# Optimization experiments

Measured on AMD Instinct MI355X. Metric: run time of the kernel, lower is better.

## Reference

```python
import jax, jax.numpy as jnp
import numpy as np

N_NODES = 2176
N_IN = 64
N_HID = 2048
N_OUT = 64
NODE_DIM = 64
HEADS = 4


def _build_edge_index():
    hs, os_ = N_IN, N_IN + N_HID
    # input -> hidden block (order: for i: for h)
    s1 = np.repeat(np.arange(0, N_IN), N_HID)
    t1 = np.tile(np.arange(hs, os_), N_IN)
    # hidden -> output block (order: for h: for o)
    s2 = np.repeat(np.arange(hs, os_), N_OUT)
    t2 = np.tile(np.arange(os_, N_NODES), N_HID)
    return jnp.asarray(np.stack([np.concatenate([s1, s2]), np.concatenate([t1, t2])]), dtype=jnp.int32)


def setup_inputs() -> dict:
    key = jax.random.key(0)
    ks = jax.random.split(key, 20)
    D, H = NODE_DIM, HEADS
    edge_index = _build_edge_index()  # [2, E]
    E = edge_index.shape[1]

    def xavier(k, shape):
        fan_in, fan_out = shape[0], shape[1]
        lim = float(np.sqrt(6.0 / (fan_in + fan_out)))
        return jax.random.uniform(k, shape, jnp.float32, -lim, lim)

    return {
        "x_input": jax.random.normal(ks[0], (N_IN,), jnp.float32),
        "node_features": jax.random.normal(ks[1], (N_NODES, D), jnp.float32) * 0.1,
        "edge_weights": jax.random.normal(ks[2], (E, 1), jnp.float32) * 0.1,
        "edge_index": edge_index,
        "wq1": xavier(ks[3], (D, D * H)), "wk1": xavier(ks[4], (D, D * H)),
        "wv1": xavier(ks[5], (D, D * H)), "we1": xavier(ks[6], (1, H)),
        "wo1": xavier(ks[7], (D * H, D)), "bo1": jnp.zeros((D,), jnp.float32),
        "wq2": xavier(ks[8], (D, D * H)), "wk2": xavier(ks[9], (D, D * H)),
        "wv2": xavier(ks[10], (D, D * H)), "we2": xavier(ks[11], (1, H)),
        "wo2": xavier(ks[12], (D * H, D)), "bo2": jnp.zeros((D,), jnp.float32),
        "wproj": xavier(ks[13], (D, 1)), "bproj": jnp.zeros((1,), jnp.float32),
        "num_output_nodes": N_OUT,
    }


def _message_pass(x, edge_index, ew, wq, wk, wv, we, wo, bo):
    # x: [N, D_in]; edge_index: [2, E]; ew: [E, 1]
    src, tgt = edge_index[0], edge_index[1]
    dout = wo.shape[1]
    heads = wq.shape[1] // dout
    q = (x[tgt] @ wq).reshape(-1, heads, dout)  # [E, H, D]
    k = (x[src] @ wk).reshape(-1, heads, dout)
    v = (x[src] @ wv).reshape(-1, heads, dout)
    attn = (q * k).sum(-1) / jnp.sqrt(jnp.float32(dout)) + ew @ we  # [E, H]
    # NOTE: the per-target segment-softmax in the torch source is dead code;
    # the effective math is leaky_relu then a global softmax over edges.
    attn = jax.nn.leaky_relu(attn, negative_slope=0.2)
    attn = jax.nn.softmax(attn, axis=0)
    weighted_v = (attn[:, :, None] * v).reshape(-1, heads * dout)  # [E, H*D]
    out = jax.ops.segment_sum(weighted_v, tgt, num_segments=x.shape[0])  # [N, H*D]
    out = out @ wo + bo
    return out + x  # residual (in_channels == out_channels)


def reference(x_input, node_features, edge_weights, edge_index,
              wq1, wk1, wv1, we1, wo1, bo1,
              wq2, wk2, wv2, we2, wo2, bo2,
              wproj, bproj, num_output_nodes):
    n_in = x_input.shape[0]
    x = node_features.at[:n_in, 0].set(x_input)
    x = jax.nn.relu(_message_pass(x, edge_index, edge_weights, wq1, wk1, wv1, we1, wo1, bo1))
    x = jax.nn.relu(_message_pass(x, edge_index, edge_weights, wq2, wk2, wv2, we2, wo2, bo2))
    out_nodes = x[x.shape[0] - num_output_nodes:]
    output = jax.nn.sigmoid(out_nodes @ wproj + bproj).squeeze()
    return output, x
```

## Files before the change

kernel.cpp:

```cpp
#include <hip/hip_runtime.h>
#include <math.h>

#define E1 131072

__device__ __forceinline__ void gemm_nn_acc(const float* __restrict__ A,
                                            const float* __restrict__ B,
                                            float acc[4][4], int tr, int tc) {
  for (int k4 = 0; k4 < 16; ++k4) {
    float4 b0 = *(const float4*)&B[(k4 * 4 + 0) * 68 + tc * 4];
    float4 b1 = *(const float4*)&B[(k4 * 4 + 1) * 68 + tc * 4];
    float4 b2 = *(const float4*)&B[(k4 * 4 + 2) * 68 + tc * 4];
    float4 b3 = *(const float4*)&B[(k4 * 4 + 3) * 68 + tc * 4];
#pragma unroll
    for (int a = 0; a < 4; ++a) {
      float4 av = *(const float4*)&A[(tr + 16 * a) * 68 + k4 * 4];
      acc[a][0] += av.x * b0.x + av.y * b1.x + av.z * b2.x + av.w * b3.x;
      acc[a][1] += av.x * b0.y + av.y * b1.y + av.z * b2.y + av.w * b3.y;
      acc[a][2] += av.x * b0.z + av.y * b1.z + av.z * b2.z + av.w * b3.z;
      acc[a][3] += av.x * b0.w + av.y * b1.w + av.z * b2.w + av.w * b3.w;
    }
  }
}

__device__ __forceinline__ void gemm_nt_acc(const float* __restrict__ A,
                                            const float* __restrict__ B,
                                            float acc[4][4], int tr, int tc) {
  for (int k4 = 0; k4 < 16; ++k4) {
    float4 av[4], bv[4];
#pragma unroll
    for (int a = 0; a < 4; ++a) av[a] = *(const float4*)&A[(tr + 16 * a) * 68 + k4 * 4];
#pragma unroll
    for (int b = 0; b < 4; ++b) bv[b] = *(const float4*)&B[(tc + 16 * b) * 68 + k4 * 4];
#pragma unroll
    for (int a = 0; a < 4; ++a)
#pragma unroll
      for (int b = 0; b < 4; ++b)
        acc[a][b] += av[a].x * bv[b].x + av[a].y * bv[b].y +
                     av[a].z * bv[b].z + av[a].w * bv[b].w;
  }
}

__device__ __forceinline__ void st_tile(float* __restrict__ C, const float acc[4][4],
                                        int tr, int tc) {
#pragma unroll
  for (int a = 0; a < 4; ++a)
    *(float4*)&C[(tr + 16 * a) * 68 + tc * 4] =
        make_float4(acc[a][0], acc[a][1], acc[a][2], acc[a][3]);
}

__device__ __forceinline__ void ld_x(float* __restrict__ dst, const float* __restrict__ src,
                                     int tid, bool sub, const float* __restrict__ xinp) {
  for (int t4 = tid; t4 < 1024; t4 += 256) {
    int r = t4 >> 4, c0 = (t4 & 15) * 4;
    float4 v = *(const float4*)(src + t4 * 4);
    if (sub && c0 == 0) v.x = xinp[r];
    *(float4*)&dst[r * 68 + c0] = v;
  }
}

__device__ __forceinline__ void ld_w(float* __restrict__ dst, const float* __restrict__ w,
                                     int h, int tid) {
  for (int t4 = tid; t4 < 1024; t4 += 256) {
    int k = t4 >> 4, c0 = (t4 & 15) * 4;
    *(float4*)&dst[k * 68 + c0] = *(const float4*)(w + k * 256 + h * 64 + c0);
  }
}

__global__ __launch_bounds__(256) void k_attn1(const float* __restrict__ x,
                                               const float* __restrict__ xinp,
                                               const float* __restrict__ wq1,
                                               const float* __restrict__ wk1,
                                               const float* __restrict__ we1,
                                               const float* __restrict__ ew,
                                               const float* __restrict__ wq2,
                                               const float* __restrict__ wk2,
                                               const float* __restrict__ wv1,
                                               const float* __restrict__ wo1,
                                               const float* __restrict__ wv2,
                                               const float* __restrict__ wo2,
                                               float* __restrict__ AggH,
                                               float* __restrict__ part,
                                               float* __restrict__ bsum,
                                               float* __restrict__ Mb,
                                               float* __restrict__ W2b) {
  __shared__ float A[4352];
  __shared__ float B[4352];
  __shared__ float C[4352];
  __shared__ float D[4352];
  __shared__ float Ew[4352];
  __shared__ float F[4352];
  __shared__ float G[4352];
  __shared__ float wred[4];
  const int bid = blockIdx.x, tid = threadIdx.x;
  const bool r1 = bid < 128;
  const int tile = (r1 ? bid : bid - 128) >> 2;
  const int h = bid & 3;
  const int j0 = tile * 64;
  const int rowSrc = r1 ? 0 : (64 + j0);
  const int rowQ = r1 ? (64 + j0) : 2112;
  const int tr = tid >> 4, tc = tid & 15;
  const float weh = we1[h];

  ld_x(A, x + rowSrc * 64, tid, r1, xinp);
  ld_x(B, x + rowQ * 64, tid, false, nullptr);
  ld_w(Ew, wk1, h, tid);
  ld_w(F, wq1, h, tid);
  if (r1) {
    for (int t4 = tid; t4 < 1024; t4 += 256) {
      int i = t4 >> 4, jl0 = (t4 & 15) * 4;
      *(float4*)&G[i * 68 + jl0] = *(const float4*)(ew + i * 2048 + j0 + jl0);
    }
  } else {
    for (int t4 = tid; t4 < 1024; t4 += 256) {
      int jl = t4 >> 4, o0 = (t4 & 15) * 4;
      *(float4*)&G[jl * 68 + o0] = *(const float4*)(ew + E1 + (j0 + jl) * 64 + o0);
    }
  }
  __syncthreads();

  {
    float kt[4][4];
#pragma unroll
    for (int a = 0; a < 4; ++a)
#pragma unroll
      for (int q = 0; q < 4; ++q) kt[a][q] = 0.f;
    gemm_nn_acc(A, Ew, kt, tr, tc);
    st_tile(C, kt, tr, tc);
    float qt[4][4];
#pragma unroll
    for (int a = 0; a < 4; ++a)
#pragma unroll
      for (int q = 0; q < 4; ++q) qt[a][q] = 0.f;
    gemm_nn_acc(B, F, qt, tr, tc);
    st_tile(D, qt, tr, tc);
  }
  __syncthreads();

  float acc[4][4];
#pragma unroll
  for (int a = 0; a < 4; ++a)
#pragma unroll
    for (int b = 0; b < 4; ++b) acc[a][b] = 0.f;
  gemm_nt_acc(D, C, acc, tr, tc);
  float esum = 0.f;
#pragma unroll
  for (int a = 0; a < 4; ++a) {
    int row = tr + 16 * a;
#pragma unroll
    for (int b = 0; b < 4; ++b) {
      int col = tc + 16 * b;
      float v = acc[a][b] * 0.125f + G[col * 68 + row] * weh;
      v = (v >= 0.f) ? v : 0.2f * v;
      v = fminf(v, 60.f);
      float e = __expf(v);
      esum += e;
      B[row * 68 + col] = e;
    }
  }
#pragma unroll
  for (int s = 1; s < 64; s <<= 1) esum += __shfl_xor(esum, s);
  if ((tid & 63) == 0) wred[tid >> 6] = esum;
  __syncthreads();

  float u[4][4];
#pragma unroll
  for (int a = 0; a < 4; ++a)
#pragma unroll
    for (int q = 0; q < 4; ++q) u[a][q] = 0.f;
  gemm_nn_acc(B, A, u, tr, tc);
  if (r1) {
#pragma unroll
    for (int a = 0; a < 4; ++a)
      *(float4*)&AggH[(j0 + tr + 16 * a) * 256 + h * 64 + tc * 4] =
          make_float4(u[a][0], u[a][1], u[a][2], u[a][3]);
  } else {
#pragma unroll
    for (int a = 0; a < 4; ++a)
      *(float4*)&part[tile * 16384 + (tr + 16 * a) * 256 + h * 64 + tc * 4] =
          make_float4(u[a][0], u[a][1], u[a][2], u[a][3]);
  }
  if (tid == 0) bsum[bid] = (wred[0] + wred[1]) + (wred[2] + wred[3]);

  if (bid < 12) {
    __syncthreads();
    const int type = bid >> 2, hh = bid & 3;
    if (type == 0) {
      for (int t4 = tid; t4 < 1024; t4 += 256) {
        int r = t4 >> 4, c0 = (t4 & 15) * 4;
        *(float4*)&A[r * 68 + c0] = *(const float4*)(wq2 + r * 256 + hh * 64 + c0);
        *(float4*)&B[r * 68 + c0] = *(const float4*)(wk2 + r * 256 + hh * 64 + c0);
      }
      __syncthreads();
      float m[4][4];
#pragma unroll
      for (int a = 0; a < 4; ++a)
#pragma unroll
        for (int b = 0; b < 4; ++b) m[a][b] = 0.f;
      gemm_nt_acc(A, B, m, tr, tc);
#pragma unroll
      for (int a = 0; a < 4; ++a)
#pragma unroll
        for (int b = 0; b < 4; ++b)
          Mb[hh * 4096 + (tr + 16 * a) * 64 + tc + 16 * b] = m[a][b];
    } else {
      const float* wv = (type == 1) ? wv1 : wv2;
      const float* wo = (type == 1) ? wo1 : wo2;
      for (int t4 = tid; t4 < 1024; t4 += 256) {
        int r = t4 >> 4, c0 = (t4 & 15) * 4;
        *(float4*)&A[r * 68 + c0] = *(const float4*)(wv + r * 256 + hh * 64 + c0);
        *(float4*)&B[r * 68 + c0] = *(const float4*)(wo + (hh * 64 + r) * 64 + c0);
      }
      __syncthreads();
      float m[4][4];
#pragma unroll
      for (int a = 0; a < 4; ++a)
#pragma unroll
        for (int b = 0; b < 4; ++b) m[a][b] = 0.f;
      gemm_nn_acc(A, B, m, tr, tc);
      float* o = W2b + (type - 1) * 16384;
#pragma unroll
      for (int a = 0; a < 4; ++a)
        *(float4*)&o[(hh * 64 + tr + 16 * a) * 64 + tc * 4] =
            make_float4(m[a][0], m[a][1], m[a][2], m[a][3]);
    }
  }
}

__global__ __launch_bounds__(256) void k_attn2(const float* __restrict__ x,
                                               const float* __restrict__ Mb,
                                               const float* __restrict__ we,
                                               const float* __restrict__ ew,
                                               float* __restrict__ AggH,
                                               float* __restrict__ part,
                                               float* __restrict__ bsum) {
  __shared__ float A[4352];
  __shared__ float B[4352];
  __shared__ float C[4352];
  __shared__ float D[4352];
  __shared__ float Em[4352];
  __shared__ float wred[4];
  const int bid = blockIdx.x, tid = threadIdx.x;
  const bool r1 = bid < 128;
  const int tile = (r1 ? bid : bid - 128) >> 2;
  const int h = bid & 3;
  const int j0 = tile * 64;
  const int rowSrc = r1 ? 0 : (64 + j0);
  const int rowQ = r1 ? (64 + j0) : 2112;
  const int tr = tid >> 4, tc = tid & 15;
  const float weh = we[h];
  const float* Mh = Mb + h * 4096;

  ld_x(A, x + rowSrc * 64, tid, false, nullptr);
  ld_x(B, x + rowQ * 64, tid, false, nullptr);
  for (int t4 = tid; t4 < 1024; t4 += 256) {
    int r = t4 >> 4, c0 = (t4 & 15) * 4;
    *(float4*)&Em[r * 68 + c0] = *(const float4*)(Mh + r * 64 + c0);
  }
  if (r1) {
    for (int t4 = tid; t4 < 1024; t4 += 256) {
      int i = t4 >> 4, jl0 = (t4 & 15) * 4;
      *(float4*)&D[i * 68 + jl0] = *(const float4*)(ew + i * 2048 + j0 + jl0);
    }
  } else {
    for (int t4 = tid; t4 < 1024; t4 += 256) {
      int jl = t4 >> 4, o0 = (t4 & 15) * 4;
      *(float4*)&D[jl * 68 + o0] = *(const float4*)(ew + E1 + (j0 + jl) * 64 + o0);
    }
  }
  __syncthreads();

  {
    float t_[4][4];
#pragma unroll
    for (int a = 0; a < 4; ++a)
#pragma unroll
      for (int q = 0; q < 4; ++q) t_[a][q] = 0.f;
    gemm_nn_acc(B, Em, t_, tr, tc);
    st_tile(C, t_, tr, tc);
  }
  __syncthreads();

  float acc[4][4];
#pragma unroll
  for (int a = 0; a < 4; ++a)
#pragma unroll
    for (int b = 0; b < 4; ++b) acc[a][b] = 0.f;
  gemm_nt_acc(C, A, acc, tr, tc);
  float esum = 0.f;
#pragma unroll
  for (int a = 0; a < 4; ++a) {
    int row = tr + 16 * a;
#pragma unroll
    for (int b = 0; b < 4; ++b) {
      int col = tc + 16 * b;
      float v = acc[a][b] * 0.125f + D[col * 68 + row] * weh;
      v = (v >= 0.f) ? v : 0.2f * v;
      v = fminf(v, 60.f);
      float e = __expf(v);
      esum += e;
      B[row * 68 + col] = e;
    }
  }
#pragma unroll
  for (int s = 1; s < 64; s <<= 1) esum += __shfl_xor(esum, s);
  if ((tid & 63) == 0) wred[tid >> 6] = esum;
  __syncthreads();

  float u[4][4];
#pragma unroll
  for (int a = 0; a < 4; ++a)
#pragma unroll
    for (int q = 0; q < 4; ++q) u[a][q] = 0.f;
  gemm_nn_acc(B, A, u, tr, tc);
  if (r1) {
#pragma unroll
    for (int a = 0; a < 4; ++a)
      *(float4*)&AggH[(j0 + tr + 16 * a) * 256 + h * 64 + tc * 4] =
          make_float4(u[a][0], u[a][1], u[a][2], u[a][3]);
  } else {
#pragma unroll
    for (int a = 0; a < 4; ++a)
      *(float4*)&part[tile * 16384 + (tr + 16 * a) * 256 + h * 64 + tc * 4] =
          make_float4(u[a][0], u[a][1], u[a][2], u[a][3]);
  }
  if (tid == 0) bsum[bid] = (wred[0] + wred[1]) + (wred[2] + wred[3]);
}

template<bool SUB, bool HEAD>
__global__ __launch_bounds__(256) void k_proj(const float* __restrict__ xin,
                                              const float* __restrict__ xinp,
                                              const float* __restrict__ AggH,
                                              const float* __restrict__ part,
                                              const float* __restrict__ bsum,
                                              const float* __restrict__ W2,
                                              const float* __restrict__ bo,
                                              const float* __restrict__ wproj,
                                              const float* __restrict__ bproj,
                                              float* __restrict__ xout,
                                              float* __restrict__ outh) {
  __shared__ float As[4][260];
  const int bid = blockIdx.x, tid = threadIdx.x;
  const int n0 = bid * 4;
  const int nl = tid >> 6, d = tid & 63;
  const int node = n0 + nl;

  float inv[4];
  {
    int l = tid & 63;
#pragma unroll
    for (int hh = 0; hh < 4; ++hh) {
      float s = (l < 32) ? bsum[l * 4 + hh] : bsum[128 + (l - 32) * 4 + hh];
#pragma unroll
      for (int st = 1; st < 64; st <<= 1) s += __shfl_xor(s, st);
      inv[hh] = 1.f / s;
    }
  }

  float xres = xin[node * 64 + d];
  if (SUB) {
    if (d == 0 && node < 64) xres = xinp[node];
  }

  float val;
  if (n0 < 64) {
    val = xres + bo[d];
  } else {
    if (n0 < 2112) {
      int a = tid >> 6, c0 = (tid & 63) * 4;
      float4 v = *(const float4*)&AggH[(n0 - 64 + a) * 256 + c0];
      float iv = inv[c0 >> 6];
      *(float4*)&As[a][c0] = make_float4(v.x * iv, v.y * iv, v.z * iv, v.w * iv);
    } else {
      int a = tid >> 6, c0 = (tid & 63) * 4;
      float4 s = make_float4(0.f, 0.f, 0.f, 0.f);
      for (int ch = 0; ch < 32; ++ch) {
        float4 v = *(const float4*)&part[ch * 16384 + (n0 - 2112 + a) * 256 + c0];
        s.x += v.x; s.y += v.y; s.z += v.z; s.w += v.w;
      }
      float iv = inv[c0 >> 6];
      *(float4*)&As[a][c0] = make_float4(s.x * iv, s.y * iv, s.z * iv, s.w * iv);
    }
    __syncthreads();
    float acc = xres + bo[d];
    for (int c4 = 0; c4 < 64; ++c4) {
      float4 a4 = *(const float4*)&As[nl][c4 * 4];
      acc += a4.x * W2[(c4 * 4 + 0) * 64 + d] + a4.y * W2[(c4 * 4 + 1) * 64 + d] +
             a4.z * W2[(c4 * 4 + 2) * 64 + d] + a4.w * W2[(c4 * 4 + 3) * 64 + d];
    }
    val = acc;
  }
  val = fmaxf(val, 0.f);
  xout[node * 64 + d] = val;

  if (HEAD) {
    if (n0 >= 2112) {
      float wv = val * wproj[d];
#pragma unroll
      for (int st = 1; st < 64; st <<= 1) wv += __shfl_xor(wv, st);
      if ((tid & 63) == 0) outh[node - 2112] = 1.f / (1.f + __expf(-(wv + bproj[0])));
    }
  }
}

extern "C" void kernel_launch(void* const* d_in, const int* in_sizes, int n_in,
                              void* d_out, int out_size, void* d_ws, size_t ws_size,
                              hipStream_t stream) {
  const float* x_input       = (const float*)d_in[0];
  const float* node_features = (const float*)d_in[1];
  const float* edge_weights  = (const float*)d_in[2];
  const float* wq1 = (const float*)d_in[4];
  const float* wk1 = (const float*)d_in[5];
  const float* wv1 = (const float*)d_in[6];
  const float* we1 = (const float*)d_in[7];
  const float* wo1 = (const float*)d_in[8];
  const float* bo1 = (const float*)d_in[9];
  const float* wq2 = (const float*)d_in[10];
  const float* wk2 = (const float*)d_in[11];
  const float* wv2 = (const float*)d_in[12];
  const float* we2 = (const float*)d_in[13];
  const float* wo2 = (const float*)d_in[14];
  const float* bo2 = (const float*)d_in[15];
  const float* wproj = (const float*)d_in[16];
  const float* bproj = (const float*)d_in[17];

  float* out = (float*)d_out;
  float* ws = (float*)d_ws;
  float* xB   = ws;
  float* AggH = xB + 139264;
  float* part = AggH + 524288;
  float* bsum = part + 524288;
  float* Mb   = bsum + 256;
  float* W2b  = Mb + 16384;

  k_attn1<<<256, 256, 0, stream>>>(node_features, x_input, wq1, wk1, we1, edge_weights,
                                   wq2, wk2, wv1, wo1, wv2, wo2,
                                   AggH, part, bsum, Mb, W2b);
  k_proj<true, false><<<544, 256, 0, stream>>>(node_features, x_input, AggH, part, bsum,
                                               W2b, bo1, nullptr, nullptr, xB, nullptr);
  k_attn2<<<256, 256, 0, stream>>>(xB, Mb, we2, edge_weights, AggH, part, bsum);
  k_proj<false, true><<<544, 256, 0, stream>>>(xB, nullptr, AggH, part, bsum,
                                               W2b + 16384, bo2, wproj, bproj, out + 64, out);
}
```

Baseline: 58.15 us.

## Halve hidden-node tile size to double attention blocks and read weights from global

The attention kernels now tile 32 hidden nodes per block instead of 64, which doubles the grid from 256 to 512 blocks so more of the GPU's compute units are busy. Weight matrices (wq/wk/Mb) are read directly from global memory inside the GEMM rather than staged in LDS, and the shared arrays are merged into one smaller buffer, cutting LDS use per block to raise occupancy. In exchange, k_proj must reduce 64 partial chunks instead of 32, partial-sum workspace doubles, and global weight reads may repeat across threads.

```diff
diff --git a/kernel.cpp b/kernel.cpp
--- a/kernel.cpp
+++ b/kernel.cpp
@@ -3,16 +3,17 @@
 
 #define E1 131072
 
-__device__ __forceinline__ void gemm_nn_acc(const float* __restrict__ A,
+template<int AR, int K4>
+__device__ __forceinline__ void gemm_nn_lds(const float* __restrict__ A,
                                             const float* __restrict__ B,
-                                            float acc[4][4], int tr, int tc) {
-  for (int k4 = 0; k4 < 16; ++k4) {
+                                            float acc[AR][4], int tr, int tc) {
+  for (int k4 = 0; k4 < K4; ++k4) {
     float4 b0 = *(const float4*)&B[(k4 * 4 + 0) * 68 + tc * 4];
     float4 b1 = *(const float4*)&B[(k4 * 4 + 1) * 68 + tc * 4];
     float4 b2 = *(const float4*)&B[(k4 * 4 + 2) * 68 + tc * 4];
     float4 b3 = *(const float4*)&B[(k4 * 4 + 3) * 68 + tc * 4];
 #pragma unroll
-    for (int a = 0; a < 4; ++a) {
+    for (int a = 0; a < AR; ++a) {
       float4 av = *(const float4*)&A[(tr + 16 * a) * 68 + k4 * 4];
       acc[a][0] += av.x * b0.x + av.y * b1.x + av.z * b2.x + av.w * b3.x;
       acc[a][1] += av.x * b0.y + av.y * b1.y + av.z * b2.y + av.w * b3.y;
@@ -22,48 +23,52 @@
   }
 }
 
-__device__ __forceinline__ void gemm_nt_acc(const float* __restrict__ A,
+template<int AR, int K4>
+__device__ __forceinline__ void gemm_nn_g(const float* __restrict__ A,
+                                          const float* __restrict__ Bg, int ldb,
+                                          float acc[AR][4], int tr, int tc) {
+  for (int k4 = 0; k4 < K4; ++k4) {
+    float4 b0 = *(const float4*)(Bg + (k4 * 4 + 0) * ldb + tc * 4);
+    float4 b1 = *(const float4*)(Bg + (k4 * 4 + 1) * ldb + tc * 4);
+    float4 b2 = *(const float4*)(Bg + (k4 * 4 + 2) * ldb + tc * 4);
+    float4 b3 = *(const float4*)(Bg + (k4 * 4 + 3) * ldb + tc * 4);
+#pragma unroll
+    for (int a = 0; a < AR; ++a) {
+      float4 av = *(const float4*)&A[(tr + 16 * a) * 68 + k4 * 4];
+      acc[a][0] += av.x * b0.x + av.y * b1.x + av.z * b2.x + av.w * b3.x;
+      acc[a][1] += av.x * b0.y + av.y * b1.y + av.z * b2.y + av.w * b3.y;
+      acc[a][2] += av.x * b0.z + av.y * b1.z + av.z * b2.z + av.w * b3.z;
+      acc[a][3] += av.x * b0.w + av.y * b1.w + av.z * b2.w + av.w * b3.w;
+    }
+  }
+}
+
+template<int AR, int BR>
+__device__ __forceinline__ void gemm_nt_lds(const float* __restrict__ A,
                                             const float* __restrict__ B,
-                                            float acc[4][4], int tr, int tc) {
+                                            float acc[AR][BR], int tr, int tc) {
   for (int k4 = 0; k4 < 16; ++k4) {
-    float4 av[4], bv[4];
-#pragma unroll
-    for (int a = 0; a < 4; ++a) av[a] = *(const float4*)&A[(tr + 16 * a) * 68 + k4 * 4];
-#pragma unroll
-    for (int b = 0; b < 4; ++b) bv[b] = *(const float4*)&B[(tc + 16 * b) * 68 + k4 * 4];
-#pragma unroll
-    for (int a = 0; a < 4; ++a)
-#pragma unroll
-      for (int b = 0; b < 4; ++b)
+    float4 av[AR], bv[BR];
+#pragma unroll
+    for (int a = 0; a < AR; ++a) av[a] = *(const float4*)&A[(tr + 16 * a) * 68 + k4 * 4];
+#pragma unroll
+    for (int b = 0; b < BR; ++b) bv[b] = *(const float4*)&B[(tc + 16 * b) * 68 + k4 * 4];
+#pragma unroll
+    for (int a = 0; a < AR; ++a)
+#pragma unroll
+      for (int b = 0; b < BR; ++b)
         acc[a][b] += av[a].x * bv[b].x + av[a].y * bv[b].y +
                      av[a].z * bv[b].z + av[a].w * bv[b].w;
   }
 }
 
-__device__ __forceinline__ void st_tile(float* __restrict__ C, const float acc[4][4],
+template<int AR>
+__device__ __forceinline__ void st_tile(float* __restrict__ C, const float acc[AR][4],
                                         int tr, int tc) {
 #pragma unroll
-  for (int a = 0; a < 4; ++a)
+  for (int a = 0; a < AR; ++a)
     *(float4*)&C[(tr + 16 * a) * 68 + tc * 4] =
         make_float4(acc[a][0], acc[a][1], acc[a][2], acc[a][3]);
-}
-
-__device__ __forceinline__ void ld_x(float* __restrict__ dst, const float* __restrict__ src,
-                                     int tid, bool sub, const float* __restrict__ xinp) {
-  for (int t4 = tid; t4 < 1024; t4 += 256) {
-    int r = t4 >> 4, c0 = (t4 & 15) * 4;
-    float4 v = *(const float4*)(src + t4 * 4);
-    if (sub && c0 == 0) v.x = xinp[r];
-    *(float4*)&dst[r * 68 + c0] = v;
-  }
-}
-
-__device__ __forceinline__ void ld_w(float* __restrict__ dst, const float* __restrict__ w,
-                                     int h, int tid) {
-  for (int t4 = tid; t4 < 1024; t4 += 256) {
-    int k = t4 >> 4, c0 = (t4 & 15) * 4;
-    *(float4*)&dst[k * 68 + c0] = *(const float4*)(w + k * 256 + h * 64 + c0);
-  }
 }
 
 __global__ __launch_bounds__(256) void k_attn1(const float* __restrict__ x,
@@ -83,146 +88,206 @@
                                                float* __restrict__ bsum,
                                                float* __restrict__ Mb,
                                                float* __restrict__ W2b) {
-  __shared__ float A[4352];
-  __shared__ float B[4352];
-  __shared__ float C[4352];
-  __shared__ float D[4352];
-  __shared__ float Ew[4352];
-  __shared__ float F[4352];
-  __shared__ float G[4352];
+  __shared__ float S_[17408];
   __shared__ float wred[4];
   const int bid = blockIdx.x, tid = threadIdx.x;
-  const bool r1 = bid < 128;
-  const int tile = (r1 ? bid : bid - 128) >> 2;
+  const bool r1 = bid < 256;
+  const int tile = (r1 ? bid : bid - 256) >> 2;
   const int h = bid & 3;
-  const int j0 = tile * 64;
-  const int rowSrc = r1 ? 0 : (64 + j0);
-  const int rowQ = r1 ? (64 + j0) : 2112;
+  const int j0 = tile * 32;
   const int tr = tid >> 4, tc = tid & 15;
   const float weh = we1[h];
 
-  ld_x(A, x + rowSrc * 64, tid, r1, xinp);
-  ld_x(B, x + rowQ * 64, tid, false, nullptr);
-  ld_w(Ew, wk1, h, tid);
-  ld_w(F, wq1, h, tid);
   if (r1) {
+    float* A = S_;
+    float* B = S_ + 4352;
+    float* C = S_ + 6528;
+    float* D = S_ + 10880;
+    float* G = S_ + 13056;
     for (int t4 = tid; t4 < 1024; t4 += 256) {
-      int i = t4 >> 4, jl0 = (t4 & 15) * 4;
+      int r = t4 >> 4, c0 = (t4 & 15) * 4;
+      float4 v = *(const float4*)(x + t4 * 4);
+      if (c0 == 0) v.x = xinp[r];
+      *(float4*)&A[r * 68 + c0] = v;
+    }
+    for (int t4 = tid; t4 < 512; t4 += 256) {
+      int r = t4 >> 4, c0 = (t4 & 15) * 4;
+      *(float4*)&B[r * 68 + c0] = *(const float4*)(x + (64 + j0 + r) * 64 + c0);
+    }
+    for (int t4 = tid; t4 < 512; t4 += 256) {
+      int i = t4 >> 3, jl0 = (t4 & 7) * 4;
       *(float4*)&G[i * 68 + jl0] = *(const float4*)(ew + i * 2048 + j0 + jl0);
     }
+    __syncthreads();
+    {
+      float kt[4][4];
+#pragma unroll
+      for (int a = 0; a < 4; ++a)
+#pragma unroll
+        for (int q = 0; q < 4; ++q) kt[a][q] = 0.f;
+      gemm_nn_g<4, 16>(A, wk1 + h * 64, 256, kt, tr, tc);
+      st_tile<4>(C, kt, tr, tc);
+      float qt[2][4];
+#pragma unroll
+      for (int a = 0; a < 2; ++a)
+#pragma unroll
+        for (int q = 0; q < 4; ++q) qt[a][q] = 0.f;
+      gemm_nn_g<2, 16>(B, wq1 + h * 64, 256, qt, tr, tc);
+      st_tile<2>(D, qt, tr, tc);
+    }
+    __syncthreads();
+    float lg[2][4];
+#pragma unroll
+    for (int a = 0; a < 2; ++a)
+#pragma unroll
+      for (int b = 0; b < 4; ++b) lg[a][b] = 0.f;
+    gemm_nt_lds<2, 4>(D, C, lg, tr, tc);
+    float esum = 0.f;
+#pragma unroll
+    for (int a = 0; a < 2; ++a) {
+      int row = tr + 16 * a;
+#pragma unroll
+      for (int b = 0; b < 4; ++b) {
+        int col = tc + 16 * b;
+        float v = lg[a][b] * 0.125f + G[col * 68 + row] * weh;
+        v = (v >= 0.f) ? v : 0.2f * v;
+        v = fminf(v, 60.f);
+        float e = __expf(v);
+        esum += e;
+        B[row * 68 + col] = e;
+      }
+    }
+#pragma unroll
+    for (int s = 1; s < 64; s <<= 1) esum += __shfl_xor(esum, s);
+    if ((tid & 63) == 0) wred[tid >> 6] = esum;
+    __syncthreads();
+    float u[2][4];
+#pragma unroll
+    for (int a = 0; a < 2; ++a)
+#pragma unroll
+      for (int q = 0; q < 4; ++q) u[a][q] = 0.f;
+    gemm_nn_lds<2, 16>(B, A, u, tr, tc);
+#pragma unroll
+    for (int a = 0; a < 2; ++a)
+      *(float4*)&AggH[(j0 + tr + 16 * a) * 256 + h * 64 + tc * 4] =
+          make_float4(u[a][0], u[a][1], u[a][2], u[a][3]);
+    if (tid == 0) bsum[bid] = (wred[0] + wred[1]) + (wred[2] + wred[3]);
+
+    if (bid < 12) {
+      __syncthreads();
+      const int type = bid >> 2, hh = bid & 3;
+      if (type == 0) {
+        for (int t4 = tid; t4 < 1024; t4 += 256) {
+          int k = t4 >> 4, c0 = (t4 & 15) * 4;
+          *(float4*)&A[k * 68 + c0] = *(const float4*)(wq2 + k * 256 + hh * 64 + c0);
+          *(float4*)&C[k * 68 + c0] = *(const float4*)(wk2 + k * 256 + hh * 64 + c0);
+        }
+        __syncthreads();
+        float m[4][4];
+#pragma unroll
+        for (int a = 0; a < 4; ++a)
+#pragma unroll
+          for (int b = 0; b < 4; ++b) m[a][b] = 0.f;
+        gemm_nt_lds<4, 4>(A, C, m, tr, tc);
+#pragma unroll
+        for (int a = 0; a < 4; ++a)
+#pragma unroll
+          for (int b = 0; b < 4; ++b)
+            Mb[hh * 4096 + (tr + 16 * a) * 64 + tc + 16 * b] = m[a][b];
+      } else {
+        const float* wv = (type == 1) ? wv1 : wv2;
+        const float* wo = (type == 1) ? wo1 : wo2;
+        for (int t4 = tid; t4 < 1024; t4 += 256) {
+          int k = t4 >> 4, c0 = (t4 & 15) * 4;
+          *(float4*)&A[k * 68 + c0] = *(const float4*)(wv + k * 256 + hh * 64 + c0);
+          *(float4*)&C[k * 68 + c0] = *(const float4*)(wo + (hh * 64 + k) * 64 + c0);
+        }
+        __syncthreads();
+        float m[4][4];
+#pragma unroll
+        for (int a = 0; a < 4; ++a)
+#pragma unroll
+          for (int q = 0; q < 4; ++q) m[a][q] = 0.f;
+        gemm_nn_lds<4, 16>(A, C, m, tr, tc);
+        float* o = W2b + (type - 1) * 16384;
+#pragma unroll
+        for (int a = 0; a < 4; ++a)
+          *(float4*)&o[(hh * 64 + tr + 16 * a) * 64 + tc * 4] =
+              make_float4(m[a][0], m[a][1], m[a][2], m[a][3]);
+      }
+    }
   } else {
+    float* A = S_;
+    float* B = S_ + 2176;
+    float* C = S_ + 6528;
+    float* D = S_ + 8704;
+    float* G = S_ + 13056;
+    for (int t4 = tid; t4 < 512; t4 += 256) {
+      int r = t4 >> 4, c0 = (t4 & 15) * 4;
+      *(float4*)&A[r * 68 + c0] = *(const float4*)(x + (64 + j0 + r) * 64 + c0);
+    }
     for (int t4 = tid; t4 < 1024; t4 += 256) {
+      int r = t4 >> 4, c0 = (t4 & 15) * 4;
+      *(float4*)&B[r * 68 + c0] = *(const float4*)(x + (2112 + r) * 64 + c0);
+    }
+    for (int t4 = tid; t4 < 512; t4 += 256) {
       int jl = t4 >> 4, o0 = (t4 & 15) * 4;
       *(float4*)&G[jl * 68 + o0] = *(const float4*)(ew + E1 + (j0 + jl) * 64 + o0);
     }
-  }
-  __syncthreads();
-
-  {
-    float kt[4][4];
+    __syncthreads();
+    {
+      float kt[2][4];
+#pragma unroll
+      for (int a = 0; a < 2; ++a)
+#pragma unroll
+        for (int q = 0; q < 4; ++q) kt[a][q] = 0.f;
+      gemm_nn_g<2, 16>(A, wk1 + h * 64, 256, kt, tr, tc);
+      st_tile<2>(C, kt, tr, tc);
+      float qt[4][4];
+#pragma unroll
+      for (int a = 0; a < 4; ++a)
+#pragma unroll
+        for (int q = 0; q < 4; ++q) qt[a][q] = 0.f;
+      gemm_nn_g<4, 16>(B, wq1 + h * 64, 256, qt, tr, tc);
+      st_tile<4>(D, qt, tr, tc);
+    }
+    __syncthreads();
+    float lg[4][2];
 #pragma unroll
     for (int a = 0; a < 4; ++a)
 #pragma unroll
-      for (int q = 0; q < 4; ++q) kt[a][q] = 0.f;
-    gemm_nn_acc(A, Ew, kt, tr, tc);
-    st_tile(C, kt, tr, tc);
-    float qt[4][4];
+      for (int b = 0; b < 2; ++b) lg[a][b] = 0.f;
+    gemm_nt_lds<4, 2>(D, C, lg, tr, tc);
+    float esum = 0.f;
+#pragma unroll
+    for (int a = 0; a < 4; ++a) {
+      int row = tr + 16 * a;
+#pragma unroll
+      for (int b = 0; b < 2; ++b) {
+        int col = tc + 16 * b;
+        float v = lg[a][b] * 0.125f + G[col * 68 + row] * weh;
+        v = (v >= 0.f) ? v : 0.2f * v;
+        v = fminf(v, 60.f);
+        float e = __expf(v);
+        esum += e;
+        B[row * 68 + col] = e;
+      }
+    }
+#pragma unroll
+    for (int s = 1; s < 64; s <<= 1) esum += __shfl_xor(esum, s);
+    if ((tid & 63) == 0) wred[tid >> 6] = esum;
+    __syncthreads();
+    float u[4][4];
 #pragma unroll
     for (int a = 0; a < 4; ++a)
 #pragma unroll
-      for (int q = 0; q < 4; ++q) qt[a][q] = 0.f;
-    gemm_nn_acc(B, F, qt, tr, tc);
-    st_tile(D, qt, tr, tc);
-  }
-  __syncthreads();
-
-  float acc[4][4];
-#pragma unroll
-  for (int a = 0; a < 4; ++a)
-#pragma unroll
-    for (int b = 0; b < 4; ++b) acc[a][b] = 0.f;
-  gemm_nt_acc(D, C, acc, tr, tc);
-  float esum = 0.f;
-#pragma unroll
-  for (int a = 0; a < 4; ++a) {
-    int row = tr + 16 * a;
-#pragma unroll
-    for (int b = 0; b < 4; ++b) {
-      int col = tc + 16 * b;
-      float v = acc[a][b] * 0.125f + G[col * 68 + row] * weh;
-      v = (v >= 0.f) ? v : 0.2f * v;
-      v = fminf(v, 60.f);
-      float e = __expf(v);
-      esum += e;
-      B[row * 68 + col] = e;
-    }
-  }
-#pragma unroll
-  for (int s = 1; s < 64; s <<= 1) esum += __shfl_xor(esum, s);
-  if ((tid & 63) == 0) wred[tid >> 6] = esum;
-  __syncthreads();
-
-  float u[4][4];
-#pragma unroll
-  for (int a = 0; a < 4; ++a)
-#pragma unroll
-    for (int q = 0; q < 4; ++q) u[a][q] = 0.f;
-  gemm_nn_acc(B, A, u, tr, tc);
-  if (r1) {
-#pragma unroll
-    for (int a = 0; a < 4; ++a)
-      *(float4*)&AggH[(j0 + tr + 16 * a) * 256 + h * 64 + tc * 4] =
-          make_float4(u[a][0], u[a][1], u[a][2], u[a][3]);
-  } else {
+      for (int q = 0; q < 4; ++q) u[a][q] = 0.f;
+    gemm_nn_lds<4, 8>(B, A, u, tr, tc);
 #pragma unroll
     for (int a = 0; a < 4; ++a)
       *(float4*)&part[tile * 16384 + (tr + 16 * a) * 256 + h * 64 + tc * 4] =
           make_float4(u[a][0], u[a][1], u[a][2], u[a][3]);
-  }
-  if (tid == 0) bsum[bid] = (wred[0] + wred[1]) + (wred[2] + wred[3]);
-
-  if (bid < 12) {
-    __syncthreads();
-    const int type = bid >> 2, hh = bid & 3;
-    if (type == 0) {
-      for (int t4 = tid; t4 < 1024; t4 += 256) {
-        int r = t4 >> 4, c0 = (t4 & 15) * 4;
-        *(float4*)&A[r * 68 + c0] = *(const float4*)(wq2 + r * 256 + hh * 64 + c0);
-        *(float4*)&B[r * 68 + c0] = *(const float4*)(wk2 + r * 256 + hh * 64 + c0);
-      }
-      __syncthreads();
-      float m[4][4];
-#pragma unroll
-      for (int a = 0; a < 4; ++a)
-#pragma unroll
-        for (int b = 0; b < 4; ++b) m[a][b] = 0.f;
-      gemm_nt_acc(A, B, m, tr, tc);
-#pragma unroll
-      for (int a = 0; a < 4; ++a)
-#pragma unroll
-        for (int b = 0; b < 4; ++b)
-          Mb[hh * 4096 + (tr + 16 * a) * 64 + tc + 16 * b] = m[a][b];
-    } else {
-      const float* wv = (type == 1) ? wv1 : wv2;
-      const float* wo = (type == 1) ? wo1 : wo2;
-      for (int t4 = tid; t4 < 1024; t4 += 256) {
-        int r = t4 >> 4, c0 = (t4 & 15) * 4;
-        *(float4*)&A[r * 68 + c0] = *(const float4*)(wv + r * 256 + hh * 64 + c0);
-        *(float4*)&B[r * 68 + c0] = *(const float4*)(wo + (hh * 64 + r) * 64 + c0);
-      }
-      __syncthreads();
-      float m[4][4];
-#pragma unroll
-      for (int a = 0; a < 4; ++a)
-#pragma unroll
-        for (int b = 0; b < 4; ++b) m[a][b] = 0.f;
-      gemm_nn_acc(A, B, m, tr, tc);
-      float* o = W2b + (type - 1) * 16384;
-#pragma unroll
-      for (int a = 0; a < 4; ++a)
-        *(float4*)&o[(hh * 64 + tr + 16 * a) * 64 + tc * 4] =
-            make_float4(m[a][0], m[a][1], m[a][2], m[a][3]);
-    }
+    if (tid == 0) bsum[bid] = (wred[0] + wred[1]) + (wred[2] + wred[3]);
   }
 }
 
@@ -233,97 +298,146 @@
                                                float* __restrict__ AggH,
                                                float* __restrict__ part,
                                                float* __restrict__ bsum) {
-  __shared__ float A[4352];
-  __shared__ float B[4352];
-  __shared__ float C[4352];
-  __shared__ float D[4352];
-  __shared__ float Em[4352];
+  __shared__ float S_[13056];
   __shared__ float wred[4];
   const int bid = blockIdx.x, tid = threadIdx.x;
-  const bool r1 = bid < 128;
-  const int tile = (r1 ? bid : bid - 128) >> 2;
+  const bool r1 = bid < 256;
+  const int tile = (r1 ? bid : bid - 256) >> 2;
   const int h = bid & 3;
-  const int j0 = tile * 64;
-  const int rowSrc = r1 ? 0 : (64 + j0);
-  const int rowQ = r1 ? (64 + j0) : 2112;
+  const int j0 = tile * 32;
   const int tr = tid >> 4, tc = tid & 15;
   const float weh = we[h];
   const float* Mh = Mb + h * 4096;
 
-  ld_x(A, x + rowSrc * 64, tid, false, nullptr);
-  ld_x(B, x + rowQ * 64, tid, false, nullptr);
-  for (int t4 = tid; t4 < 1024; t4 += 256) {
-    int r = t4 >> 4, c0 = (t4 & 15) * 4;
-    *(float4*)&Em[r * 68 + c0] = *(const float4*)(Mh + r * 64 + c0);
-  }
   if (r1) {
+    float* A = S_;
+    float* B = S_ + 4352;
+    float* C = S_ + 6528;
+    float* G = S_ + 8704;
     for (int t4 = tid; t4 < 1024; t4 += 256) {
-      int i = t4 >> 4, jl0 = (t4 & 15) * 4;
-      *(float4*)&D[i * 68 + jl0] = *(const float4*)(ew + i * 2048 + j0 + jl0);
-    }
-  } else {
-    for (int t4 = tid; t4 < 1024; t4 += 256) {
-      int jl = t4 >> 4, o0 = (t4 & 15) * 4;
-      *(float4*)&D[jl * 68 + o0] = *(const float4*)(ew + E1 + (j0 + jl) * 64 + o0);
-    }
-  }
-  __syncthreads();
-
-  {
-    float t_[4][4];
-#pragma unroll
-    for (int a = 0; a < 4; ++a)
-#pragma unroll
-      for (int q = 0; q < 4; ++q) t_[a][q] = 0.f;
-    gemm_nn_acc(B, Em, t_, tr, tc);
-    st_tile(C, t_, tr, tc);
-  }
-  __syncthreads();
-
-  float acc[4][4];
-#pragma unroll
-  for (int a = 0; a < 4; ++a)
-#pragma unroll
-    for (int b = 0; b < 4; ++b) acc[a][b] = 0.f;
-  gemm_nt_acc(C, A, acc, tr, tc);
-  float esum = 0.f;
-#pragma unroll
-  for (int a = 0; a < 4; ++a) {
-    int row = tr + 16 * a;
-#pragma unroll
-    for (int b = 0; b < 4; ++b) {
-      int col = tc + 16 * b;
-      float v = acc[a][b] * 0.125f + D[col * 68 + row] * weh;
-      v = (v >= 0.f) ? v : 0.2f * v;
-      v = fminf(v, 60.f);
-      float e = __expf(v);
-      esum += e;
-      B[row * 68 + col] = e;
-    }
-  }
-#pragma unroll
-  for (int s = 1; s < 64; s <<= 1) esum += __shfl_xor(esum, s);
-  if ((tid & 63) == 0) wred[tid >> 6] = esum;
-  __syncthreads();
-
-  float u[4][4];
-#pragma unroll
-  for (int a = 0; a < 4; ++a)
-#pragma unroll
-    for (int q = 0; q < 4; ++q) u[a][q] = 0.f;
-  gemm_nn_acc(B, A, u, tr, tc);
-  if (r1) {
-#pragma unroll
-    for (int a = 0; a < 4; ++a)
+      int r = t4 >> 4, c0 = (t4 & 15) * 4;
+      *(float4*)&A[r * 68 + c0] = *(const float4*)(x + t4 * 4);
+    }
+    for (int t4 = tid; t4 < 512; t4 += 256) {
+      int r = t4 >> 4, c0 = (t4 & 15) * 4;
+      *(float4*)&B[r * 68 + c0] = *(const float4*)(x + (64 + j0 + r) * 64 + c0);
+    }
+    for (int t4 = tid; t4 < 512; t4 += 256) {
+      int i = t4 >> 3, jl0 = (t4 & 7) * 4;
+      *(float4*)&G[i * 68 + jl0] = *(const float4*)(ew + i * 2048 + j0 + jl0);
+    }
+    __syncthreads();
+    {
+      float t_[2][4];
+#pragma unroll
+      for (int a = 0; a < 2; ++a)
+#pragma unroll
+        for (int q = 0; q < 4; ++q) t_[a][q] = 0.f;
+      gemm_nn_g<2, 16>(B, Mh, 64, t_, tr, tc);
+      st_tile<2>(C, t_, tr, tc);
+    }
+    __syncthreads();
+    float lg[2][4];
+#pragma unroll
+    for (int a = 0; a < 2; ++a)
+#pragma unroll
+      for (int b = 0; b < 4; ++b) lg[a][b] = 0.f;
+    gemm_nt_lds<2, 4>(C, A, lg, tr, tc);
+    float esum = 0.f;
+#pragma unroll
+    for (int a = 0; a < 2; ++a) {
+      int row = tr + 16 * a;
+#pragma unroll
+      for (int b = 0; b < 4; ++b) {
+        int col = tc + 16 * b;
+        float v = lg[a][b] * 0.125f + G[col * 68 + row] * weh;
+        v = (v >= 0.f) ? v : 0.2f * v;
+        v = fminf(v, 60.f);
+        float e = __expf(v);
+        esum += e;
+        B[row * 68 + col] = e;
+      }
+    }
+#pragma unroll
+    for (int s = 1; s < 64; s <<= 1) esum += __shfl_xor(esum, s);
+    if ((tid & 63) == 0) wred[tid >> 6] = esum;
+    __syncthreads();
+    float u[2][4];
+#pragma unroll
+    for (int a = 0; a < 2; ++a)
+#pragma unroll
+      for (int q = 0; q < 4; ++q) u[a][q] = 0.f;
+    gemm_nn_lds<2, 16>(B, A, u, tr, tc);
+#pragma unroll
+    for (int a = 0; a < 2; ++a)
       *(float4*)&AggH[(j0 + tr + 16 * a) * 256 + h * 64 + tc * 4] =
           make_float4(u[a][0], u[a][1], u[a][2], u[a][3]);
+    if (tid == 0) bsum[bid] = (wred[0] + wred[1]) + (wred[2] + wred[3]);
   } else {
+    float* A = S_;
+    float* B = S_ + 2176;
+    float* C = S_ + 6528;
+    float* G = S_ + 10880;
+    for (int t4 = tid; t4 < 512; t4 += 256) {
+      int r = t4 >> 4, c0 = (t4 & 15) * 4;
+      *(float4*)&A[r * 68 + c0] = *(const float4*)(x + (64 + j0 + r) * 64 + c0);
+    }
+    for (int t4 = tid; t4 < 1024; t4 += 256) {
+      int r = t4 >> 4, c0 = (t4 & 15) * 4;
+      *(float4*)&B[r * 68 + c0] = *(const float4*)(x + (2112 + r) * 64 + c0);
+    }
+    for (int t4 = tid; t4 < 512; t4 += 256) {
+      int jl = t4 >> 4, o0 = (t4 & 15) * 4;
+      *(float4*)&G[jl * 68 + o0] = *(const float4*)(ew + E1 + (j0 + jl) * 64 + o0);
+    }
+    __syncthreads();
+    {
+      float t_[4][4];
+#pragma unroll
+      for (int a = 0; a < 4; ++a)
+#pragma unroll
+        for (int q = 0; q < 4; ++q) t_[a][q] = 0.f;
+      gemm_nn_g<4, 16>(B, Mh, 64, t_, tr, tc);
+      st_tile<4>(C, t_, tr, tc);
+    }
+    __syncthreads();
+    float lg[4][2];
+#pragma unroll
+    for (int a = 0; a < 4; ++a)
+#pragma unroll
+      for (int b = 0; b < 2; ++b) lg[a][b] = 0.f;
+    gemm_nt_lds<4, 2>(C, A, lg, tr, tc);
+    float esum = 0.f;
+#pragma unroll
+    for (int a = 0; a < 4; ++a) {
+      int row = tr + 16 * a;
+#pragma unroll
+      for (int b = 0; b < 2; ++b) {
+        int col = tc + 16 * b;
+        float v = lg[a][b] * 0.125f + G[col * 68 + row] * weh;
+        v = (v >= 0.f) ? v : 0.2f * v;
+        v = fminf(v, 60.f);
+        float e = __expf(v);
+        esum += e;
+        B[row * 68 + col] = e;
+      }
+    }
+#pragma unroll
+    for (int s = 1; s < 64; s <<= 1) esum += __shfl_xor(esum, s);
+    if ((tid & 63) == 0) wred[tid >> 6] = esum;
+    __syncthreads();
+    float u[4][4];
+#pragma unroll
+    for (int a = 0; a < 4; ++a)
+#pragma unroll
+      for (int q = 0; q < 4; ++q) u[a][q] = 0.f;
+    gemm_nn_lds<4, 8>(B, A, u, tr, tc);
 #pragma unroll
     for (int a = 0; a < 4; ++a)
       *(float4*)&part[tile * 16384 + (tr + 16 * a) * 256 + h * 64 + tc * 4] =
           make_float4(u[a][0], u[a][1], u[a][2], u[a][3]);
-  }
-  if (tid == 0) bsum[bid] = (wred[0] + wred[1]) + (wred[2] + wred[3]);
+    if (tid == 0) bsum[bid] = (wred[0] + wred[1]) + (wred[2] + wred[3]);
+  }
 }
 
 template<bool SUB, bool HEAD>
@@ -349,7 +463,7 @@
     int l = tid & 63;
 #pragma unroll
     for (int hh = 0; hh < 4; ++hh) {
-      float s = (l < 32) ? bsum[l * 4 + hh] : bsum[128 + (l - 32) * 4 + hh];
+      float s = bsum[4 * l + hh] + bsum[256 + 4 * l + hh];
 #pragma unroll
       for (int st = 1; st < 64; st <<= 1) s += __shfl_xor(s, st);
       inv[hh] = 1.f / s;
@@ -373,7 +487,7 @@
     } else {
       int a = tid >> 6, c0 = (tid & 63) * 4;
       float4 s = make_float4(0.f, 0.f, 0.f, 0.f);
-      for (int ch = 0; ch < 32; ++ch) {
+      for (int ch = 0; ch < 64; ++ch) {
         float4 v = *(const float4*)&part[ch * 16384 + (n0 - 2112 + a) * 256 + c0];
         s.x += v.x; s.y += v.y; s.z += v.z; s.w += v.w;
       }
@@ -428,16 +542,16 @@
   float* xB   = ws;
   float* AggH = xB + 139264;
   float* part = AggH + 524288;
-  float* bsum = part + 524288;
-  float* Mb   = bsum + 256;
+  float* bsum = part + 1048576;
+  float* Mb   = bsum + 512;
   float* W2b  = Mb + 16384;
 
-  k_attn1<<<256, 256, 0, stream>>>(node_features, x_input, wq1, wk1, we1, edge_weights,
+  k_attn1<<<512, 256, 0, stream>>>(node_features, x_input, wq1, wk1, we1, edge_weights,
                                    wq2, wk2, wv1, wo1, wv2, wo2,
                                    AggH, part, bsum, Mb, W2b);
   k_proj<true, false><<<544, 256, 0, stream>>>(node_features, x_input, AggH, part, bsum,
                                                W2b, bo1, nullptr, nullptr, xB, nullptr);
-  k_attn2<<<256, 256, 0, stream>>>(xB, Mb, we2, edge_weights, AggH, part, bsum);
+  k_attn2<<<512, 256, 0, stream>>>(xB, Mb, we2, edge_weights, AggH, part, bsum);
   k_proj<false, true><<<544, 256, 0, stream>>>(xB, nullptr, AggH, part, bsum,
                                                W2b + 16384, bo2, wproj, bproj, out + 64, out);
 }
```

New measurement: 63.60 us. +9.4%, slower.
